# Performance work log

Hardware: AMD Instinct MI355X
Metric: run time of the kernel (lower is better)

## Reference

```python
import jax, jax.numpy as jnp
import numpy as np

POOL_SIZES = [(5, 10), (3, 6), (2, 4)]
P_VALUE = 1e-8
EVAL_T = 0.03


def _pool_up(k, p0, p1):
    # avg_pool2d with kernel=stride=(H/p0, W/p1), padding 0 (exact divisibility),
    # followed by repeat_interleave upsampling back to (B,H,W,D).
    B, H, W, D = k.shape
    kh, kw = H // p0, W // p1
    pooled = k.reshape(B, p0, kh, p1, kw, D).mean(axis=(2, 4))  # (B,p0,p1,D)
    up = jnp.broadcast_to(pooled[:, :, None, :, None, :], (B, p0, kh, p1, kw, D))
    return up.reshape(B, H, W, D)


def setup_inputs() -> dict:
    key = jax.random.key(0)
    ks = jax.random.split(key, 7)
    B, H, W, D = 64, 30, 60, 64
    x = jax.random.normal(ks[0], (B, H, W, D), dtype=jnp.float32)
    qk_w = jax.random.normal(ks[1], (2 * D, D), dtype=jnp.float32) * 0.02
    qk_b = jax.random.normal(ks[2], (2 * D,), dtype=jnp.float32) * 0.02
    score_w = jax.random.normal(ks[3], (1, 3), dtype=jnp.float32) * 0.5
    score_b = jax.random.normal(ks[4], (1,), dtype=jnp.float32) * 0.5
    noise_x = jax.random.uniform(ks[5], (B, H * W, 1), dtype=jnp.float32)
    noise_r = jax.random.uniform(ks[6], (B, H * W, 1), dtype=jnp.float32)
    return {"x": x, "qk_w": qk_w, "qk_b": qk_b, "score_w": score_w,
            "score_b": score_b, "noise_x": noise_x, "noise_r": noise_r}


def reference(x, qk_w, qk_b, score_w, score_b, noise_x, noise_r):
    B, H, W, D = x.shape
    scale = D ** (-0.5)
    qk = x @ qk_w.T + qk_b                      # (B,H,W,2D)
    q, k = qk[..., :D], qk[..., D:]             # (B,H,W,D)
    # attn[:,0,1:] only uses row 0 (original q) vs pooled k columns 1..3.
    scores = jnp.stack(
        [jnp.sum(q * _pool_up(k, p0, p1), axis=-1) for (p0, p1) in POOL_SIZES],
        axis=-1) * scale                        # (B,H,W,3)
    attn = scores @ score_w.T + score_b         # (B,H,W,1)
    attn = attn.reshape(B, H * W, 1)
    attn_soft = jax.nn.sigmoid(attn)
    # gumbel-sigmoid (eval mode, T = 0.03)
    gx = jnp.log(attn_soft + P_VALUE)
    gr = jnp.log(1.0 - attn_soft + P_VALUE)
    nx = -jnp.log(-jnp.log(noise_x + P_VALUE) + P_VALUE)
    nr = -jnp.log(-jnp.log(noise_r + P_VALUE) + P_VALUE)
    gx = (gx + nx) / (EVAL_T + P_VALUE)
    gr = (gr + nr) / (EVAL_T + P_VALUE)
    logits = jnp.concatenate([gx, gr], axis=-1)  # (B,HW,2)
    mask = jax.nn.softmax(logits, axis=-1)[..., 0:1]  # (B,HW,1)
    return mask
```

## Files before the change

kernel.cpp:

```cpp
#include <hip/hip_runtime.h>
#include <math.h>

#define BB 64
#define HH 30
#define WW 60
#define DD 64
#define NPIX 1800
#define NREG 76

__constant__ int c_rowband[HH] = {0,0,0,0,0,0, 1,1,1,1, 2,2, 3,3,3, 4,4,4, 5,5, 6,6,6,6, 7,7,7,7,7,7};
__constant__ int c_colband[WW] = {0,0,0,0,0,0, 1,1,1,1, 2,2, 3,3,3, 4,4,4, 5,5, 6,6,6,6, 7,7,7,7,7,7,
                                  8,8,8,8,8,8, 9,9,9,9, 10,10, 11,11,11, 12,12,12, 13,13, 14,14,14,14, 15,15,15,15,15,15};
__constant__ int c_s0col[16] = {0,1,1,2,2,3,3,4,5,6,6,7,7,8,8,9};
__constant__ int c_s1col[16] = {0,0,1,1,1,1,2,2,3,3,4,4,4,4,5,5};
__constant__ int c_s0row[8] = {0,1,1,2,2,3,3,4};
__constant__ int c_s1row[8] = {0,0,1,1,1,1,2,2};

__global__ __launch_bounds__(256) void ka_pool(
    const float* __restrict__ x, const float* __restrict__ qk_w,
    const float* __restrict__ qk_b, float* __restrict__ psum,
    float* __restrict__ ET_ws, float* __restrict__ u_ws,
    float* __restrict__ v_ws, float* __restrict__ s_ws)
{
    const int t = threadIdx.x;

    if (blockIdx.x >= BB * HH) {
        const int e = blockIdx.x - BB * HH;
        if (t < 64) {
            float acc = 0.f;
#pragma unroll 8
            for (int jj = 0; jj < 64; ++jj)
                acc += qk_w[jj * 64 + t] * qk_w[(64 + jj) * 64 + e];
            ET_ws[e * 64 + t] = acc;
        } else if (e == 0 && t >= 64 && t < 128) {
            const int d = t - 64;
            float acc = 0.f;
            for (int jj = 0; jj < 64; ++jj) acc += qk_w[jj * 64 + d] * qk_b[64 + jj];
            u_ws[d] = acc;
        } else if (e == 0 && t >= 128 && t < 192) {
            const int e2 = t - 128;
            float acc = 0.f;
            for (int jj = 0; jj < 64; ++jj) acc += qk_w[(64 + jj) * 64 + e2] * qk_b[jj];
            v_ws[e2] = acc;
        } else if (e == 0 && t == 192) {
            float acc = 0.f;
            for (int jj = 0; jj < 64; ++jj) acc += qk_b[jj] * qk_b[64 + jj];
            s_ws[0] = acc;
        }
        return;
    }

    const int b = blockIdx.x / HH;
    const int h = blockIdx.x % HH;
    const int j = t & 63;
    const int g = t >> 6;

    const float* xrow = x + ((size_t)(b * NPIX + h * WW) + g * 15) * DD;
    float v[15];
#pragma unroll
    for (int i = 0; i < 15; ++i) v[i] = xrow[i * DD + j];

    float a0, a1, a2, a3;
    if ((g & 1) == 0) {
        a0 = ((v[0]+v[1])+(v[2]+v[3]))+(v[4]+v[5]);
        a1 = (v[6]+v[7])+(v[8]+v[9]);
        a2 = v[10]+v[11];
        a3 = (v[12]+v[13])+v[14];
    } else {
        a0 = (v[0]+v[1])+v[2];
        a1 = v[3]+v[4];
        a2 = (v[5]+v[6])+(v[7]+v[8]);
        a3 = ((v[9]+v[10])+(v[11]+v[12]))+(v[13]+v[14]);
    }

    const float s0m = a1 + a2;
    const float s10 = a0 + a1;
    const float s11 = a2 + a3;
    const float s2  = s10 + s11;

    const int r0 = (h / 6) * 10;
    const int r1 = 50 + (h / 10) * 6;
    const int r2 = 68 + (h / 15) * 4;
    const int c0a = c_s0col[4*g], c0b = c_s0col[4*g+1], c0c = c_s0col[4*g+3];
    const int c1a = c_s1col[4*g], c1b = c_s1col[4*g+2];

    float* pb = psum + (size_t)b * NREG * 64 + j;
    atomicAdd(pb + (r0 + c0a) * 64, a0);
    atomicAdd(pb + (r0 + c0b) * 64, s0m);
    atomicAdd(pb + (r0 + c0c) * 64, a3);
    atomicAdd(pb + (r1 + c1a) * 64, s10);
    atomicAdd(pb + (r1 + c1b) * 64, s11);
    atomicAdd(pb + (r2 + g) * 64, s2);
}

__global__ __launch_bounds__(256) void kb_G(
    const float* __restrict__ score_w, const float* __restrict__ score_b,
    const float* __restrict__ psum, const float* __restrict__ ET_ws,
    const float* __restrict__ u_ws, const float* __restrict__ v_ws,
    const float* __restrict__ s_ws, float* __restrict__ G, float* __restrict__ cc)
{
    __shared__ float ETs[4096];
    __shared__ float XC[16 * 64];
    __shared__ float ul[64], vl[64];

    const int b = blockIdx.x >> 3;
    const int rb = blockIdx.x & 7;
    const int t = threadIdx.x;
    const int lane = t & 63;
    const int g = t >> 6;

    for (int i = t; i < 4096; i += 256) ETs[i] = ET_ws[i];
    if (t < 64) ul[t] = u_ws[t];
    else if (t < 128) vl[t - 64] = v_ws[t - 64];

    const float w0n = score_w[0] * (1.0f / 36.0f);
    const float w1n = score_w[1] * (1.0f / 100.0f);
    const float w2n = score_w[2] * (1.0f / 225.0f);
    const float* pb = psum + (size_t)b * NREG * 64;
    const int r0 = 10 * c_s0row[rb];
    const int r1 = 50 + 6 * c_s1row[rb];
    const int r2 = 68 + 4 * (rb >> 2);
    for (int i = t; i < 16 * 64; i += 256) {
        const int cb = i >> 6, d = i & 63;
        XC[i] = w0n * pb[(r0 + c_s0col[cb]) * 64 + d]
              + w1n * pb[(r1 + c_s1col[cb]) * 64 + d]
              + w2n * pb[(r2 + (cb >> 2)) * 64 + d];
    }
    __syncthreads();

    float et[64];
#pragma unroll
    for (int e = 0; e < 64; ++e) et[e] = ETs[e * 64 + lane];

    const float wsum = score_w[0] + score_w[1] + score_w[2];
    const float sv = s_ws[0];
    const float sb = score_b[0];
    const float uval = ul[lane];
    const float vval = vl[lane];

#pragma unroll
    for (int ci = 0; ci < 4; ++ci) {
        const int cb = g * 4 + ci;
        const float4* xc4 = (const float4*)(XC + cb * 64);
        float acc = 0.f;
#pragma unroll
        for (int q = 0; q < 16; ++q) {
            const float4 xv = xc4[q];
            acc += xv.x * et[4*q] + xv.y * et[4*q+1] + xv.z * et[4*q+2] + xv.w * et[4*q+3];
        }
        G[(size_t)b * 8192 + rb * 1024 + cb * 64 + lane] = 0.125f * (acc + wsum * uval);

        float pv = vval * XC[cb * 64 + lane];
        pv += __shfl_xor(pv, 1, 64);  pv += __shfl_xor(pv, 2, 64);
        pv += __shfl_xor(pv, 4, 64);  pv += __shfl_xor(pv, 8, 64);
        pv += __shfl_xor(pv, 16, 64); pv += __shfl_xor(pv, 32, 64);
        if (lane == 0) cc[b * 128 + rb * 16 + cb] = 0.125f * (pv + wsum * sv) + sb;
    }
}

__global__ __launch_bounds__(256) void kc_mask(
    const float* __restrict__ x, const float* __restrict__ G,
    const float* __restrict__ cc, const float* __restrict__ noise_x,
    const float* __restrict__ noise_r, float* __restrict__ out)
{
    __shared__ float Grow[1024];
    __shared__ float crow[16];
    __shared__ float attnv[64];
    __shared__ int cbt[64];

    const int b = blockIdx.x / HH;
    const int h = blockIdx.x % HH;
    const int t = threadIdx.x;
    const int lane = t & 63;
    const int g = t >> 6;
    const int rb = c_rowband[h];

    ((float4*)Grow)[t] = ((const float4*)(G + (size_t)b * 8192 + rb * 1024))[t];
    if (t < 16) crow[t] = cc[b * 128 + rb * 16 + t];
    if (t < 60) cbt[t] = c_colband[t];
    __syncthreads();

    const float4* x4 = (const float4*)(x + (size_t)(b * NPIX + h * WW) * DD);
    const int f = lane & 15;
    const int pg = lane >> 4;
#pragma unroll
    for (int i = 0; i < 4; ++i) {
        const int pl = i * 4 + pg;
        if (pl < 15) {
            const int p = g * 15 + pl;
            const int cb = cbt[p];
            const float4 xv = x4[p * 16 + f];
            const float4 gv = ((const float4*)Grow)[cb * 16 + f];
            float s = xv.x * gv.x + xv.y * gv.y + xv.z * gv.z + xv.w * gv.w;
            s += __shfl_xor(s, 1, 64);
            s += __shfl_xor(s, 2, 64);
            s += __shfl_xor(s, 4, 64);
            s += __shfl_xor(s, 8, 64);
            if (f == 0) attnv[p] = s + crow[cb];
        }
    }
    __syncthreads();

    if (t < 60) {
        const int pix = b * NPIX + h * WW + t;
        const float a = attnv[t];
        const float sg = 1.0f / (1.0f + expf(-a));
        const float gx = logf(sg + 1e-8f);
        const float gr = logf(1.0f - sg + 1e-8f);
        const float ux = noise_x[pix];
        const float ur = noise_r[pix];
        const float nx = -logf(-logf(ux + 1e-8f) + 1e-8f);
        const float nr = -logf(-logf(ur + 1e-8f) + 1e-8f);
        const float INV_T = 1.0f / (0.03f + 1e-8f);
        const float A = (gx + nx) * INV_T;
        const float R = (gr + nr) * INV_T;
        out[pix] = 1.0f / (1.0f + expf(R - A));
    }
}

extern "C" void kernel_launch(void* const* d_in, const int* in_sizes, int n_in,
                              void* d_out, int out_size, void* d_ws, size_t ws_size,
                              hipStream_t stream)
{
    const float* x       = (const float*)d_in[0];
    const float* qk_w    = (const float*)d_in[1];
    const float* qk_b    = (const float*)d_in[2];
    const float* score_w = (const float*)d_in[3];
    const float* score_b = (const float*)d_in[4];
    const float* noise_x = (const float*)d_in[5];
    const float* noise_r = (const float*)d_in[6];
    float* out = (float*)d_out;

    float* psum  = (float*)d_ws;
    float* G     = psum + (size_t)BB * NREG * 64;
    float* cc    = G + (size_t)BB * 128 * 64;
    float* ET_ws = cc + BB * 128;
    float* u_ws  = ET_ws + 4096;
    float* v_ws  = u_ws + 64;
    float* s_ws  = v_ws + 64;

    hipMemsetAsync(psum, 0, (size_t)BB * NREG * 64 * sizeof(float), stream);
    ka_pool<<<BB * HH + 64, 256, 0, stream>>>(x, qk_w, qk_b, psum, ET_ws, u_ws, v_ws, s_ws);
    kb_G<<<BB * 8, 256, 0, stream>>>(score_w, score_b, psum, ET_ws, u_ws, v_ws, s_ws, G, cc);
    kc_mask<<<BB * HH, 256, 0, stream>>>(x, G, cc, noise_x, noise_r, out);
}
```

Before: 109.7 us.

## Replace atomic pooled sums with per-row band sums reduced in the G kernel

The pooling kernel now writes per-row, per-column-band partial sums with plain stores instead of issuing atomicAdds into a zeroed pooled-sum buffer. The second kernel then reduces the relevant rows into three pool levels in shared memory and combines the column bands into the weighted XC vectors. This drops the memset launch and the atomic contention. In exchange it writes a larger intermediate buffer (per row instead of per region) and adds redundant row reads in kb_G, since the 8 row-band blocks of a batch each re-read their overlapping row ranges.

```diff
diff --git a/kernel.cpp b/kernel.cpp
--- a/kernel.cpp
+++ b/kernel.cpp
@@ -6,7 +6,6 @@
 #define WW 60
 #define DD 64
 #define NPIX 1800
-#define NREG 76
 
 __constant__ int c_rowband[HH] = {0,0,0,0,0,0, 1,1,1,1, 2,2, 3,3,3, 4,4,4, 5,5, 6,6,6,6, 7,7,7,7,7,7};
 __constant__ int c_colband[WW] = {0,0,0,0,0,0, 1,1,1,1, 2,2, 3,3,3, 4,4,4, 5,5, 6,6,6,6, 7,7,7,7,7,7,
@@ -15,10 +14,14 @@
 __constant__ int c_s1col[16] = {0,0,1,1,1,1,2,2,3,3,4,4,4,4,5,5};
 __constant__ int c_s0row[8] = {0,1,1,2,2,3,3,4};
 __constant__ int c_s1row[8] = {0,0,1,1,1,1,2,2};
-
-__global__ __launch_bounds__(256) void ka_pool(
+__constant__ int c_s0st[16] = {0,1,1,3,3,5,5,7,8,9,9,11,11,13,13,15};
+__constant__ int c_s0ct[16] = {1,2,2,2,2,2,2,1,1,2,2,2,2,2,2,1};
+__constant__ int c_s1st[16] = {0,0,2,2,2,2,6,6,8,8,10,10,10,10,14,14};
+__constant__ int c_s1ct[16] = {2,2,4,4,4,4,2,2,2,2,4,4,4,4,2,2};
+
+__global__ __launch_bounds__(256) void ka_rowsum(
     const float* __restrict__ x, const float* __restrict__ qk_w,
-    const float* __restrict__ qk_b, float* __restrict__ psum,
+    const float* __restrict__ qk_b, float* __restrict__ rowsum,
     float* __restrict__ ET_ws, float* __restrict__ u_ws,
     float* __restrict__ v_ws, float* __restrict__ s_ws)
 {
@@ -73,33 +76,23 @@
         a3 = ((v[9]+v[10])+(v[11]+v[12]))+(v[13]+v[14]);
     }
 
-    const float s0m = a1 + a2;
-    const float s10 = a0 + a1;
-    const float s11 = a2 + a3;
-    const float s2  = s10 + s11;
-
-    const int r0 = (h / 6) * 10;
-    const int r1 = 50 + (h / 10) * 6;
-    const int r2 = 68 + (h / 15) * 4;
-    const int c0a = c_s0col[4*g], c0b = c_s0col[4*g+1], c0c = c_s0col[4*g+3];
-    const int c1a = c_s1col[4*g], c1b = c_s1col[4*g+2];
-
-    float* pb = psum + (size_t)b * NREG * 64 + j;
-    atomicAdd(pb + (r0 + c0a) * 64, a0);
-    atomicAdd(pb + (r0 + c0b) * 64, s0m);
-    atomicAdd(pb + (r0 + c0c) * 64, a3);
-    atomicAdd(pb + (r1 + c1a) * 64, s10);
-    atomicAdd(pb + (r1 + c1b) * 64, s11);
-    atomicAdd(pb + (r2 + g) * 64, s2);
+    float* rs = rowsum + ((size_t)(b * HH + h) * 16 + 4 * g) * 64 + j;
+    rs[0]   = a0;
+    rs[64]  = a1;
+    rs[128] = a2;
+    rs[192] = a3;
 }
 
 __global__ __launch_bounds__(256) void kb_G(
     const float* __restrict__ score_w, const float* __restrict__ score_b,
-    const float* __restrict__ psum, const float* __restrict__ ET_ws,
+    const float* __restrict__ rowsum, const float* __restrict__ ET_ws,
     const float* __restrict__ u_ws, const float* __restrict__ v_ws,
     const float* __restrict__ s_ws, float* __restrict__ G, float* __restrict__ cc)
 {
     __shared__ float ETs[4096];
+    __shared__ float S0L[1024];
+    __shared__ float S1L[1024];
+    __shared__ float S2L[1024];
     __shared__ float XC[16 * 64];
     __shared__ float ul[64], vl[64];
 
@@ -113,18 +106,46 @@
     if (t < 64) ul[t] = u_ws[t];
     else if (t < 128) vl[t - 64] = v_ws[t - 64];
 
-    const float w0n = score_w[0] * (1.0f / 36.0f);
-    const float w1n = score_w[1] * (1.0f / 100.0f);
-    const float w2n = score_w[2] * (1.0f / 225.0f);
-    const float* pb = psum + (size_t)b * NREG * 64;
-    const int r0 = 10 * c_s0row[rb];
-    const int r1 = 50 + 6 * c_s1row[rb];
-    const int r2 = 68 + 4 * (rb >> 2);
-    for (int i = t; i < 16 * 64; i += 256) {
-        const int cb = i >> 6, d = i & 63;
-        XC[i] = w0n * pb[(r0 + c_s0col[cb]) * 64 + d]
-              + w1n * pb[(r1 + c_s1col[cb]) * 64 + d]
-              + w2n * pb[(r2 + (cb >> 2)) * 64 + d];
+    const int s0r = c_s0row[rb], s1r = c_s1row[rb], s2r = rb >> 2;
+    const int h00 = 6 * s0r,  h01 = h00 + 6;
+    const int h10 = 10 * s1r, h11 = h10 + 10;
+    const int h20 = 15 * s2r, h21 = h20 + 15;
+    int hmin = h00 < h10 ? h00 : h10; if (h20 < hmin) hmin = h20;
+    int hmax = h01 > h11 ? h01 : h11; if (h21 > hmax) hmax = h21;
+
+    float4 a0 = {0.f,0.f,0.f,0.f}, a1 = {0.f,0.f,0.f,0.f}, a2 = {0.f,0.f,0.f,0.f};
+    const float4* rsb = (const float4*)(rowsum + (size_t)b * HH * 1024);
+    for (int h = hmin; h < hmax; ++h) {
+        const float4 rv = rsb[h * 256 + t];
+        if (h >= h00 && h < h01) { a0.x += rv.x; a0.y += rv.y; a0.z += rv.z; a0.w += rv.w; }
+        if (h >= h10 && h < h11) { a1.x += rv.x; a1.y += rv.y; a1.z += rv.z; a1.w += rv.w; }
+        if (h >= h20 && h < h21) { a2.x += rv.x; a2.y += rv.y; a2.z += rv.z; a2.w += rv.w; }
+    }
+    ((float4*)S0L)[t] = a0;
+    ((float4*)S1L)[t] = a1;
+    ((float4*)S2L)[t] = a2;
+    __syncthreads();
+
+    {
+        const float w0n = score_w[0] * (1.0f / 36.0f);
+        const float w1n = score_w[1] * (1.0f / 100.0f);
+        const float w2n = score_w[2] * (1.0f / 225.0f);
+        const int cb = (4 * t) >> 6;
+        const int d0 = (4 * t) & 63;
+        const int st0 = c_s0st[cb], ct0 = c_s0ct[cb];
+        const int st1 = c_s1st[cb], ct1 = c_s1ct[cb];
+        const int st2 = cb & ~3;
+#pragma unroll
+        for (int k = 0; k < 4; ++k) {
+            const int d = d0 + k;
+            float s0v = 0.f;
+            for (int c = 0; c < ct0; ++c) s0v += S0L[(st0 + c) * 64 + d];
+            float s1v = 0.f;
+            for (int c = 0; c < ct1; ++c) s1v += S1L[(st1 + c) * 64 + d];
+            const float s2v = S2L[st2 * 64 + d] + S2L[(st2 + 1) * 64 + d]
+                            + S2L[(st2 + 2) * 64 + d] + S2L[(st2 + 3) * 64 + d];
+            XC[cb * 64 + d] = w0n * s0v + w1n * s1v + w2n * s2v;
+        }
     }
     __syncthreads();
 
@@ -231,16 +252,15 @@
     const float* noise_r = (const float*)d_in[6];
     float* out = (float*)d_out;
 
-    float* psum  = (float*)d_ws;
-    float* G     = psum + (size_t)BB * NREG * 64;
-    float* cc    = G + (size_t)BB * 128 * 64;
-    float* ET_ws = cc + BB * 128;
-    float* u_ws  = ET_ws + 4096;
-    float* v_ws  = u_ws + 64;
-    float* s_ws  = v_ws + 64;
-
-    hipMemsetAsync(psum, 0, (size_t)BB * NREG * 64 * sizeof(float), stream);
-    ka_pool<<<BB * HH + 64, 256, 0, stream>>>(x, qk_w, qk_b, psum, ET_ws, u_ws, v_ws, s_ws);
-    kb_G<<<BB * 8, 256, 0, stream>>>(score_w, score_b, psum, ET_ws, u_ws, v_ws, s_ws, G, cc);
+    float* rowsum = (float*)d_ws;
+    float* G      = rowsum + (size_t)BB * HH * 16 * 64;
+    float* cc     = G + (size_t)BB * 128 * 64;
+    float* ET_ws  = cc + BB * 128;
+    float* u_ws   = ET_ws + 4096;
+    float* v_ws   = u_ws + 64;
+    float* s_ws   = v_ws + 64;
+
+    ka_rowsum<<<BB * HH + 64, 256, 0, stream>>>(x, qk_w, qk_b, rowsum, ET_ws, u_ws, v_ws, s_ws);
+    kb_G<<<BB * 8, 256, 0, stream>>>(score_w, score_b, rowsum, ET_ws, u_ws, v_ws, s_ws, G, cc);
     kc_mask<<<BB * HH, 256, 0, stream>>>(x, G, cc, noise_x, noise_r, out);
 }
```

Result: no change. 110.0 us (+0.2%).
